# Performance work log

Hardware: AMD Instinct MI355X
Metric: run time of the kernel (lower is better)

## Reference

```python
import jax, jax.numpy as jnp
import numpy as np

L, B, S, D, H = 6, 2, 2048, 512, 8
DH = D // H
FF = 4 * D
EPS = 1e-5


def setup_inputs() -> dict:
    key = jax.random.key(0)
    ks = jax.random.split(key, 10)
    w = lambda k, shape: jax.random.normal(k, shape, jnp.float32) * 0.02
    return {
        "query": jax.random.normal(ks[0], (B, S, D), jnp.float32),
        "key": jax.random.normal(ks[1], (B, S, D), jnp.float32),
        "query_mask": jnp.ones((B, S), jnp.int32),
        "key_mask": jnp.ones((B, S), jnp.int32),
        # per-layer stacked params; conv1d(kernel=1) == linear with weight [out,in]
        "Wq": w(ks[2], (L, D, D)), "bq": jnp.zeros((L, D), jnp.float32),
        "Wk": w(ks[3], (L, D, D)), "bk": jnp.zeros((L, D), jnp.float32),
        "Wv": w(ks[4], (L, D, D)), "bv": jnp.zeros((L, D), jnp.float32),
        "Wo": w(ks[5], (L, D, D)), "bo": jnp.zeros((L, D), jnp.float32),
        "ln1_g": jnp.ones((L, D), jnp.float32), "ln1_b": jnp.zeros((L, D), jnp.float32),
        "ff_w1": w(ks[6], (L, FF, D)), "ff_b1": jnp.zeros((L, FF), jnp.float32),
        "ff_w2": w(ks[7], (L, D, FF)), "ff_b2": jnp.zeros((L, D), jnp.float32),
        "ln2_g": jnp.ones((L, D), jnp.float32), "ln2_b": jnp.zeros((L, D), jnp.float32),
    }


def _layer_norm(x, g, b):
    m = jnp.mean(x, axis=-1, keepdims=True)
    v = jnp.mean(jnp.square(x - m), axis=-1, keepdims=True)
    return (x - m) * jax.lax.rsqrt(v + EPS) * g + b


def reference(query, key, query_mask, key_mask,
              Wq, bq, Wk, bk, Wv, bv, Wo, bo,
              ln1_g, ln1_b, ff_w1, ff_b1, ff_w2, ff_b2, ln2_g, ln2_b):
    b_, s_, d_ = query.shape
    kpad = (key_mask == 0)[:, None, None, :]          # [B,1,1,K]
    qm = query_mask.astype(query.dtype)[:, :, None]    # [B,S,1]
    x = query
    for i in range(L):
        # QKV projections (conv1d kernel-size-1 == linear), split heads -> [B,H,S,DH]
        def split(t):
            return t.reshape(b_, s_, H, DH).transpose(0, 2, 1, 3)
        q = split(x @ Wq[i].T + bq[i]) * (float(DH) ** -0.5)
        k = split(key @ Wk[i].T + bk[i])
        v = split(key @ Wv[i].T + bv[i])
        attn = jnp.einsum('bhqd,bhkd->bhqk', q, k)
        attn = jnp.where(kpad, -jnp.inf, attn)
        attn = jax.nn.softmax(attn, axis=-1)
        o = jnp.einsum('bhqk,bhkd->bhqd', attn, v)
        o = o.transpose(0, 2, 1, 3).reshape(b_, s_, H * DH)
        o = (o @ Wo[i].T + bo[i]) * qm                 # output proj + query mask
        x = _layer_norm(o + x, ln1_g[i], ln1_b[i])
        h = jax.nn.leaky_relu(x @ ff_w1[i].T + ff_b1[i], 0.01)
        f = (h @ ff_w2[i].T + ff_b2[i]) * qm           # FFN mask on output
        x = _layer_norm(f + x, ln2_g[i], ln2_b[i])
    return x
```

## Files before the change

### kernel.cpp

```cpp
#include <hip/hip_runtime.h>
#include <stdint.h>

constexpr int LAYERS = 6;
constexpr int Bc = 2, Sc = 2048, Dc = 512, Hc = 8, DHc = 64, FFc = 2048;
constexpr int Mc = Bc * Sc;
constexpr int NS = 2;
constexpr int KCHUNK = Sc / NS;

typedef __attribute__((ext_vector_type(8))) __bf16 bf16x8;
typedef __attribute__((ext_vector_type(4))) __bf16 bf16x4;
typedef __attribute__((ext_vector_type(4))) float f32x4;

__device__ __forceinline__ void async_ld16(const void* g, void* lds) {
  __builtin_amdgcn_global_load_lds(
      (const __attribute__((address_space(1))) uint32_t*)g,
      (__attribute__((address_space(3))) uint32_t*)lds, 16, 0, 0);
}

__global__ __launch_bounds__(256) void cvt_all(
    const float* __restrict__ Wq, const float* __restrict__ Wo,
    const float* __restrict__ fw1, const float* __restrict__ fw2,
    const float* __restrict__ query, const float* __restrict__ key,
    __bf16* __restrict__ wq_b, __bf16* __restrict__ wo_b,
    __bf16* __restrict__ w1_b, __bf16* __restrict__ w2_b,
    __bf16* __restrict__ x_b, __bf16* __restrict__ key_b,
    float* __restrict__ x_f) {
  size_t i = ((size_t)blockIdx.x * 256 + threadIdx.x) * 4;
  constexpr size_t nW = (size_t)LAYERS * Dc * Dc;
  constexpr size_t nF = (size_t)LAYERS * FFc * Dc;
  constexpr size_t nX = (size_t)Mc * Dc;
  const float* src;
  __bf16* dst;
  float* fdst = nullptr;
  if (i < nW) { src = Wq + i; dst = wq_b + i; }
  else if (i < 2 * nW) { size_t j = i - nW; src = Wo + j; dst = wo_b + j; }
  else if (i < 2 * nW + nF) { size_t j = i - 2 * nW; src = fw1 + j; dst = w1_b + j; }
  else if (i < 2 * nW + 2 * nF) { size_t j = i - 2 * nW - nF; src = fw2 + j; dst = w2_b + j; }
  else if (i < 2 * nW + 2 * nF + nX) {
    size_t j = i - 2 * nW - 2 * nF;
    src = query + j; dst = x_b + j; fdst = x_f + j;
  } else {
    size_t j = i - 2 * nW - 2 * nF - nX;
    src = key + j; dst = key_b + j;
  }
  const float4 v = *(const float4*)src;
  bf16x4 o;
  o[0] = (__bf16)v.x; o[1] = (__bf16)v.y; o[2] = (__bf16)v.z; o[3] = (__bf16)v.w;
  *(bf16x4*)dst = o;
  if (fdst) *(float4*)fdst = v;
}

__global__ __launch_bounds__(256) void cvt_kv_kernel(const float* __restrict__ Wk,
                                                     const float* __restrict__ Wv,
                                                     __bf16* __restrict__ out) {
  size_t i = ((size_t)blockIdx.x * 256 + threadIdx.x) * 4;
  int n = (int)(i / ((size_t)Dc * Dc));
  int lyr = n >> 1, p = n & 1;
  size_t idx = i - (size_t)n * Dc * Dc;
  const float* src = (p ? Wv : Wk) + (size_t)lyr * Dc * Dc + idx;
  const float4 v = *(const float4*)src;
  bf16x4 o;
  o[0] = (__bf16)v.x; o[1] = (__bf16)v.y; o[2] = (__bf16)v.z; o[3] = (__bf16)v.w;
  *(bf16x4*)(out + i) = o;
}

__global__ __launch_bounds__(256) void kbias_kernel(const int* __restrict__ km,
                                                    float* __restrict__ kb, int n) {
  int i = blockIdx.x * 256 + threadIdx.x;
  if (i < n) kb[i] = km[i] ? 0.f : -1e30f;
}

template <int BM, int BN, int WM, int WN, int EPI>
__global__ __launch_bounds__(256) void gemm_bt(
    const __bf16* __restrict__ A, const __bf16* __restrict__ W,
    const float* __restrict__ bias, const float* __restrict__ bias2,
    float* __restrict__ outf, __bf16* __restrict__ outb,
    __bf16* __restrict__ outb2, float scale,
    int M, int N, int K, int Kstride) {
  constexpr int BK = 64;
  __shared__ __bf16 As[2][BM * BK];
  __shared__ __bf16 Bs[2][BN * BK];
  const int tid = threadIdx.x;
  const int l15 = tid & 15;
  const int lg = (tid & 63) >> 4;
  const int w = tid >> 6;
  const int wm = w >> 1, wn = w & 1;
  const int tm = blockIdx.y * BM;
  const int tn = blockIdx.x * BN;
  const int z = blockIdx.z;
  const __bf16* Ap = A + (size_t)tm * Kstride + (size_t)z * K;
  const __bf16* Wp = W + (size_t)tn * Kstride + (size_t)z * K;
  f32x4 acc[WM][WN] = {};

  auto stage = [&](int k0, int bf) {
#pragma unroll
    for (int c = 0; c < BM * 8 / 256; ++c) {
      int cc = c * 256 + tid;
      int r = cc >> 3, s = cc & 7;
      int ss = s ^ (r & 7);
      async_ld16(Ap + (size_t)r * Kstride + k0 + ss * 8, &As[bf][cc * 8]);
    }
#pragma unroll
    for (int c = 0; c < BN * 8 / 256; ++c) {
      int cc = c * 256 + tid;
      int r = cc >> 3, s = cc & 7;
      int ss = s ^ (r & 7);
      async_ld16(Wp + (size_t)r * Kstride + k0 + ss * 8, &Bs[bf][cc * 8]);
    }
  };

  const int nk = K / BK;
  stage(0, 0);
  __syncthreads();
  int buf = 0;
  for (int t = 0; t < nk; ++t) {
    if (t + 1 < nk) stage((t + 1) * BK, buf ^ 1);
    bf16x8 af[WM][2], bfr[WN][2];
#pragma unroll
    for (int i = 0; i < WM; ++i) {
      int row = wm * WM * 16 + i * 16 + l15;
#pragma unroll
      for (int kf = 0; kf < 2; ++kf)
        af[i][kf] = *(const bf16x8*)&As[buf][row * 64 + (((kf * 4 + lg) ^ (row & 7)) * 8)];
    }
#pragma unroll
    for (int j = 0; j < WN; ++j) {
      int row = wn * WN * 16 + j * 16 + l15;
#pragma unroll
      for (int kf = 0; kf < 2; ++kf)
        bfr[j][kf] = *(const bf16x8*)&Bs[buf][row * 64 + (((kf * 4 + lg) ^ (row & 7)) * 8)];
    }
#pragma unroll
    for (int kf = 0; kf < 2; ++kf)
#pragma unroll
      for (int i = 0; i < WM; ++i)
#pragma unroll
        for (int j = 0; j < WN; ++j)
          acc[i][j] = __builtin_amdgcn_mfma_f32_16x16x32_bf16(af[i][kf], bfr[j][kf], acc[i][j], 0, 0, 0);
    __syncthreads();
    buf ^= 1;
  }

  if constexpr (EPI == 6) {
    const bool isV = ((tn & 1023) >= 512);
    const int lyr = tn >> 10;
    const int b = tm >> 11;
    const int sbase = tm & (Sc - 1);
    if (isV) {
      __bf16* T = (__bf16*)&As[0][0];
#pragma unroll
      for (int i = 0; i < WM; ++i) {
#pragma unroll
        for (int j = 0; j < WN; ++j) {
          const int d = wn * WN * 16 + j * 16 + l15;
          const int dg = (tn & 511) + d;
          const float bv = bias2[lyr * 512 + dg];
          const int s0 = wm * WM * 16 + i * 16 + lg * 4;
          bf16x4 pk;
#pragma unroll
          for (int r = 0; r < 4; ++r) pk[r] = (__bf16)(acc[i][j][r] + bv);
          const int slot = (s0 >> 3) ^ (d & 7);
          *(bf16x4*)&T[d * 64 + slot * 8 + (s0 & 7)] = pk;
        }
      }
      __syncthreads();
      const int rr = tid >> 3;
      const int c8 = tid & 7;
#pragma unroll
      for (int pass = 0; pass < 4; ++pass) {
        const int d = pass * 32 + rr;
        const int slot = c8 ^ (d & 7);
        bf16x8 v8 = *(const bf16x8*)&T[d * 64 + slot * 8];
        const int dg = (tn & 511) + d;
        const int h = dg >> 6, dh = dg & 63;
        *(bf16x8*)&outb2[((((size_t)(lyr * Bc + b) * Hc + h)) * DHc + dh) * Sc +
                         sbase + c8 * 8] = v8;
      }
    } else {
#pragma unroll
      for (int i = 0; i < WM; ++i) {
#pragma unroll
        for (int j = 0; j < WN; ++j) {
          const int d = wn * WN * 16 + j * 16 + l15;
          const int dg = (tn & 511) + d;
          const float bv = bias[lyr * 512 + dg];
          const int h = dg >> 6, dh = dg & 63;
#pragma unroll
          for (int r = 0; r < 4; ++r) {
            const int s = sbase + wm * WM * 16 + i * 16 + lg * 4 + r;
            outb[((((size_t)(lyr * Bc + b) * Hc + h)) * Sc + s) * DHc + dh] =
                (__bf16)(acc[i][j][r] + bv);
          }
        }
      }
    }
    return;
  }

#pragma unroll
  for (int i = 0; i < WM; ++i) {
#pragma unroll
    for (int j = 0; j < WN; ++j) {
      const int n = tn + wn * WN * 16 + j * 16 + l15;
      float bv;
      if constexpr (EPI == 0) {
        bv = (z == 0) ? bias[n] : 0.f;
      } else {
        bv = bias[n];
      }
#pragma unroll
      for (int r = 0; r < 4; ++r) {
        const int m = tm + wm * WM * 16 + i * 16 + lg * 4 + r;
        float v = acc[i][j][r] + bv;
        if constexpr (EPI == 0) {
          outf[(size_t)z * M * N + (size_t)m * N + n] = v;
        } else if constexpr (EPI == 1) {
          int b = m >> 11, s = m & (Sc - 1);
          int h = n >> 6, dh = n & 63;
          outb[(((size_t)(b * Hc + h)) * Sc + s) * DHc + dh] = (__bf16)(v * scale);
        } else if constexpr (EPI == 4) {
          float lv = v > 0.f ? v : 0.01f * v;
          outb[(size_t)m * N + n] = (__bf16)lv;
        }
      }
    }
  }
}

__global__ __launch_bounds__(256, 5) void attn_kernel(
    const __bf16* __restrict__ q, const __bf16* __restrict__ k,
    const __bf16* __restrict__ vt, const float* __restrict__ kb,
    __bf16* __restrict__ Opart, float* __restrict__ mpart,
    float* __restrict__ lpart) {
  const int bid = blockIdx.x;
  const int o = (bid & 7) * 128 + (bid >> 3);
  const int qb = o & 31;
  const int p = o >> 5;
  const int bh = p >> 1;
  const int z = p & 1;
  const int b = bh >> 3;
  const int w = threadIdx.x >> 6;
  const int l = threadIdx.x & 63;
  const int l15 = l & 15;
  const int lg = l >> 4;
  const int tid = threadIdx.x;
  const int qbase = qb * 64 + w * 16;
  const int k0 = z * KCHUNK;

  const __bf16* qp = q + ((size_t)bh * Sc + qbase) * DHc;
  const __bf16* kp = k + (size_t)bh * Sc * DHc;
  const __bf16* vp = vt + (size_t)bh * DHc * Sc;
  const float* kbp = kb + (size_t)b * Sc;

  bf16x8 qf[2];
  qf[0] = *(const bf16x8*)(qp + l15 * DHc + lg * 8);
  qf[1] = *(const bf16x8*)(qp + l15 * DHc + 32 + lg * 8);

  bf16x8 onesf;
#pragma unroll
  for (int i = 0; i < 8; ++i) onesf[i] = (__bf16)1.0f;

  f32x4 oacc[4] = {};
  f32x4 lacc = {};
  float mr = -1e30f;

  __shared__ __bf16 Ks[2][4096];
  __shared__ __bf16 Vs[2][4096];

  auto stage = [&](int t, int bf) {
    const int kt = k0 + t * 64;
#pragma unroll
    for (int ii = 0; ii < 2; ++ii) {
      int i = ii * 256 + tid;
      int r = i >> 3;
      int bsrc = (i & 7) ^ (r & 7);
      async_ld16(kp + (size_t)(kt + r) * DHc + bsrc * 8, &Ks[bf][i * 8]);
      async_ld16(vp + (size_t)r * Sc + kt + bsrc * 8, &Vs[bf][i * 8]);
    }
  };

  stage(0, 0);
  __syncthreads();

  constexpr int NT = KCHUNK / 64;
  int buf = 0;
  for (int t = 0; t < NT; ++t) {
    const int kt = k0 + t * 64;
    if (t + 1 < NT) stage(t + 1, buf ^ 1);

    float4 mb4[4];
#pragma unroll
    for (int cb = 0; cb < 4; ++cb)
      mb4[cb] = *(const float4*)&kbp[kt + cb * 16 + lg * 4];

    f32x4 sacc[4] = {};
    __builtin_amdgcn_s_setprio(1);
#pragma unroll
    for (int kf = 0; kf < 2; ++kf) {
#pragma unroll
      for (int cb = 0; cb < 4; ++cb) {
        int row = cb * 16 + l15;
        bf16x8 kfr = *(const bf16x8*)&Ks[buf][row * 64 + (((kf * 4 + lg) ^ (row & 7)) * 8)];
        sacc[cb] = __builtin_amdgcn_mfma_f32_16x16x32_bf16(kfr, qf[kf], sacc[cb], 0, 0, 0);
      }
    }
    __builtin_amdgcn_s_setprio(0);
    sacc[0][0] += mb4[0].x; sacc[0][1] += mb4[0].y; sacc[0][2] += mb4[0].z; sacc[0][3] += mb4[0].w;
    sacc[1][0] += mb4[1].x; sacc[1][1] += mb4[1].y; sacc[1][2] += mb4[1].z; sacc[1][3] += mb4[1].w;
    sacc[2][0] += mb4[2].x; sacc[2][1] += mb4[2].y; sacc[2][2] += mb4[2].z; sacc[2][3] += mb4[2].w;
    sacc[3][0] += mb4[3].x; sacc[3][1] += mb4[3].y; sacc[3][2] += mb4[3].z; sacc[3][3] += mb4[3].w;

    float mx = sacc[0][0];
#pragma unroll
    for (int cb = 0; cb < 4; ++cb)
#pragma unroll
      for (int r = 0; r < 4; ++r) mx = fmaxf(mx, sacc[cb][r]);
    mx = fmaxf(mx, __shfl_xor(mx, 16, 64));
    mx = fmaxf(mx, __shfl_xor(mx, 32, 64));

    if (__any(mx > mr + 8.f)) {
      float mn = fmaxf(mr, mx);
      float f = __expf(mr - mn);
      mr = mn;
      float fj[4];
#pragma unroll
      for (int j = 0; j < 4; ++j) fj[j] = __shfl(f, lg * 4 + j, 64);
#pragma unroll
      for (int j = 0; j < 4; ++j) lacc[j] *= fj[j];
#pragma unroll
      for (int db = 0; db < 4; ++db)
#pragma unroll
        for (int j = 0; j < 4; ++j) oacc[db][j] *= fj[j];
    }

    unsigned pw[4][2];
#pragma unroll
    for (int cb = 0; cb < 4; ++cb) {
#pragma unroll
      for (int w2 = 0; w2 < 2; ++w2) {
        union { __bf16 h[2]; unsigned u; } cu;
        cu.h[0] = (__bf16)__expf(sacc[cb][2 * w2] - mr);
        cu.h[1] = (__bf16)__expf(sacc[cb][2 * w2 + 1] - mr);
        pw[cb][w2] = cu.u;
      }
    }

    const int srcA = ((lg & 1) * 2) * 16 + l15;
    const int srcB = srcA + 16;
    const bool hi = (lg >> 1) & 1;
#pragma unroll
    for (int kf = 0; kf < 2; ++kf) {
      unsigned t0a = __shfl((int)pw[kf * 2][0], srcA, 64);
      unsigned t0b = __shfl((int)pw[kf * 2 + 1][0], srcA, 64);
      unsigned t1a = __shfl((int)pw[kf * 2][1], srcA, 64);
      unsigned t1b = __shfl((int)pw[kf * 2 + 1][1], srcA, 64);
      unsigned t2a = __shfl((int)pw[kf * 2][0], srcB, 64);
      unsigned t2b = __shfl((int)pw[kf * 2 + 1][0], srcB, 64);
      unsigned t3a = __shfl((int)pw[kf * 2][1], srcB, 64);
      unsigned t3b = __shfl((int)pw[kf * 2 + 1][1], srcB, 64);
      union { unsigned u[4]; bf16x8 v; } pa;
      pa.u[0] = hi ? t0b : t0a;
      pa.u[1] = hi ? t1b : t1a;
      pa.u[2] = hi ? t2b : t2a;
      pa.u[3] = hi ? t3b : t3a;
      __builtin_amdgcn_s_setprio(1);
      lacc = __builtin_amdgcn_mfma_f32_16x16x32_bf16(pa.v, onesf, lacc, 0, 0, 0);
#pragma unroll
      for (int db = 0; db < 4; ++db) {
        int row = db * 16 + l15;
        bf16x8 vf = *(const bf16x8*)&Vs[buf][row * 64 + (((kf * 4 + lg) ^ (row & 7)) * 8)];
        oacc[db] = __builtin_amdgcn_mfma_f32_16x16x32_bf16(pa.v, vf, oacc[db], 0, 0, 0);
      }
      __builtin_amdgcn_s_setprio(0);
    }
    __syncthreads();
    buf ^= 1;
  }

  const size_t obase = (((size_t)(z * Bc * Hc + bh)) * Sc + qbase) * DHc;
#pragma unroll
  for (int db = 0; db < 4; ++db)
#pragma unroll
    for (int j = 0; j < 4; ++j)
      Opart[obase + (size_t)(lg * 4 + j) * DHc + db * 16 + l15] = (__bf16)oacc[db][j];
  const int row0 = (z * Bc * Hc + bh) * Sc + qbase;
  if (lg == 0) mpart[row0 + l15] = mr;
  if (l15 == 0) {
#pragma unroll
    for (int j = 0; j < 4; ++j) lpart[row0 + lg * 4 + j] = lacc[j];
  }
}

__global__ __launch_bounds__(256) void attn_combine(
    const __bf16* __restrict__ Opart, const float* __restrict__ mpart,
    const float* __restrict__ lpart, __bf16* __restrict__ out) {
  int t = blockIdx.x * 256 + threadIdx.x;
  int d = t & 63;
  int row = t >> 6;
  int bh = row >> 11, s = row & (Sc - 1);
  constexpr int RSTRIDE = Bc * Hc * Sc;
  float m0 = mpart[row], m1 = mpart[RSTRIDE + row];
  float l0 = lpart[row], l1 = lpart[RSTRIDE + row];
  float M = fmaxf(m0, m1);
  float e0 = __expf(m0 - M), e1 = __expf(m1 - M);
  float denom = e0 * l0 + e1 * l1;
  float o0 = (float)Opart[(size_t)row * DHc + d];
  float o1 = (float)Opart[((size_t)RSTRIDE + row) * DHc + d];
  float o = (e0 * o0 + e1 * o1) / denom;
  int b = bh >> 3, h = bh & 7;
  out[(((size_t)b * Sc + s)) * Dc + h * DHc + d] = (__bf16)o;
}

__global__ __launch_bounds__(256) void add_ln_kernel(
    const float* __restrict__ res, const float* __restrict__ res2,
    const int* __restrict__ rmask, const float* __restrict__ xin,
    const float* __restrict__ g, const float* __restrict__ bb,
    float* __restrict__ xo, __bf16* __restrict__ xbo) {
  const int tid = threadIdx.x;
  const int rl = tid >> 7;
  const int row = blockIdx.x * 2 + rl;
  const int ci = (tid & 127) * 4;
  const size_t base = (size_t)row * Dc + ci;
  const float4 a = *(const float4*)(res + base);
  const float4 a2 = *(const float4*)(res2 + base);
  const float4 xv = *(const float4*)(xin + base);
  const float mfac = (float)rmask[row];
  float4 v;
  v.x = (a.x + a2.x) * mfac + xv.x;
  v.y = (a.y + a2.y) * mfac + xv.y;
  v.z = (a.z + a2.z) * mfac + xv.z;
  v.w = (a.w + a2.w) * mfac + xv.w;
  float s = v.x + v.y + v.z + v.w;
#pragma unroll
  for (int d = 1; d < 64; d <<= 1) s += __shfl_xor(s, d, 64);
  __shared__ float red[4], red2[4];
  if ((tid & 63) == 0) red[tid >> 6] = s;
  __syncthreads();
  float mean = (red[rl * 2] + red[rl * 2 + 1]) * (1.0f / Dc);
  float4 dv;
  dv.x = v.x - mean; dv.y = v.y - mean; dv.z = v.z - mean; dv.w = v.w - mean;
  float qq = dv.x * dv.x + dv.y * dv.y + dv.z * dv.z + dv.w * dv.w;
#pragma unroll
  for (int d = 1; d < 64; d <<= 1) qq += __shfl_xor(qq, d, 64);
  if ((tid & 63) == 0) red2[tid >> 6] = qq;
  __syncthreads();
  float var = (red2[rl * 2] + red2[rl * 2 + 1]) * (1.0f / Dc);
  float rs = rsqrtf(var + 1e-5f);
  const float4 gv = *(const float4*)(g + ci);
  const float4 bv = *(const float4*)(bb + ci);
  float4 ov;
  ov.x = dv.x * rs * gv.x + bv.x;
  ov.y = dv.y * rs * gv.y + bv.y;
  ov.z = dv.z * rs * gv.z + bv.z;
  ov.w = dv.w * rs * gv.w + bv.w;
  *(float4*)(xo + base) = ov;
  bf16x4 ob;
  ob[0] = (__bf16)ov.x; ob[1] = (__bf16)ov.y; ob[2] = (__bf16)ov.z; ob[3] = (__bf16)ov.w;
  *(bf16x4*)(xbo + base) = ob;
}

extern "C" void kernel_launch(void* const* d_in, const int* in_sizes, int n_in,
                              void* d_out, int out_size, void* d_ws, size_t ws_size,
                              hipStream_t stream) {
  (void)in_sizes; (void)n_in; (void)out_size; (void)ws_size;
  const float* query = (const float*)d_in[0];
  const float* key   = (const float*)d_in[1];
  const int* qmask   = (const int*)d_in[2];
  const int* kmask   = (const int*)d_in[3];
  const float* Wq = (const float*)d_in[4];
  const float* bq = (const float*)d_in[5];
  const float* Wk = (const float*)d_in[6];
  const float* bk = (const float*)d_in[7];
  const float* Wv = (const float*)d_in[8];
  const float* bv = (const float*)d_in[9];
  const float* Wo = (const float*)d_in[10];
  const float* bo = (const float*)d_in[11];
  const float* ln1g = (const float*)d_in[12];
  const float* ln1b = (const float*)d_in[13];
  const float* fw1 = (const float*)d_in[14];
  const float* fb1 = (const float*)d_in[15];
  const float* fw2 = (const float*)d_in[16];
  const float* fb2 = (const float*)d_in[17];
  const float* ln2g = (const float*)d_in[18];
  const float* ln2b = (const float*)d_in[19];

  char* ws = (char*)d_ws;
  size_t off = 0;
  auto carve = [&](size_t bytes) -> void* {
    void* p = ws + off;
    off += (bytes + 255) & ~(size_t)255;
    return p;
  };
  float* x_f    = (float*)carve((size_t)Mc * Dc * 4);
  float* tmp_f  = (float*)carve((size_t)2 * Mc * Dc * 4);
  __bf16* x_b   = (__bf16*)carve((size_t)Mc * Dc * 2);
  __bf16* key_b = (__bf16*)carve((size_t)Mc * Dc * 2);
  __bf16* q_b   = (__bf16*)carve((size_t)Mc * Dc * 2);
  __bf16* at_b  = (__bf16*)carve((size_t)Mc * Dc * 2);
  __bf16* h_b   = (__bf16*)carve((size_t)Mc * FFc * 2);
  __bf16* k_all = (__bf16*)carve((size_t)LAYERS * Mc * Dc * 2);
  __bf16* vt_all= (__bf16*)carve((size_t)LAYERS * Mc * Dc * 2);
  __bf16* wq_b  = (__bf16*)carve((size_t)LAYERS * Dc * Dc * 2);
  __bf16* wkv_b = (__bf16*)carve((size_t)LAYERS * 2 * Dc * Dc * 2);
  __bf16* wo_b  = (__bf16*)carve((size_t)LAYERS * Dc * Dc * 2);
  __bf16* w1_b  = (__bf16*)carve((size_t)LAYERS * FFc * Dc * 2);
  __bf16* w2_b  = (__bf16*)carve((size_t)LAYERS * Dc * FFc * 2);
  float* ml_f   = (float*)carve((size_t)NS * Bc * Hc * Sc * 4 * 2);
  float* kb_f   = (float*)carve((size_t)Bc * Sc * 4);

  __bf16* opart_b = h_b;
  float* mpart_f = ml_f;
  float* lpart_f = ml_f + (size_t)NS * Bc * Hc * Sc;
  float* tmp2_f = tmp_f + (size_t)Mc * Dc;

  cvt_all<<<19456, 256, 0, stream>>>(Wq, Wo, fw1, fw2, query, key,
                                     wq_b, wo_b, w1_b, w2_b, x_b, key_b, x_f);
  cvt_kv_kernel<<<LAYERS * 2 * Dc * Dc / 1024, 256, 0, stream>>>(Wk, Wv, wkv_b);
  kbias_kernel<<<Bc * Sc / 256, 256, 0, stream>>>(kmask, kb_f, Bc * Sc);

  const dim3 blk(256);
  const dim3 gP64(Dc / 64, Mc / 64);
  const dim3 gOP(Dc / 64, Mc / 64, 2);
  const dim3 gFF2(Dc / 64, Mc / 64, 2);
  const dim3 gKV(LAYERS * 2 * Dc / 128, Mc / 64);
  const dim3 gFF1(FFc / 128, Mc / 64);
  const dim3 gAttn(Sc / 64 * Bc * Hc * NS);
  const dim3 gComb(Bc * Hc * Sc * DHc / 256);
  const dim3 gLN(Mc / 2);

  gemm_bt<64, 128, 2, 4, 6><<<gKV, blk, 0, stream>>>(
      key_b, wkv_b, bk, bv, nullptr, k_all, vt_all, 1.0f,
      Mc, LAYERS * 2 * Dc, Dc, Dc);

  for (int i = 0; i < LAYERS; ++i) {
    const __bf16* wq_i = wq_b + (size_t)i * Dc * Dc;
    const __bf16* wo_i = wo_b + (size_t)i * Dc * Dc;
    const __bf16* w1_i = w1_b + (size_t)i * FFc * Dc;
    const __bf16* w2_i = w2_b + (size_t)i * Dc * FFc;
    const __bf16* k_i  = k_all + (size_t)i * Mc * Dc;
    const __bf16* vt_i = vt_all + (size_t)i * Mc * Dc;

    gemm_bt<64, 64, 2, 2, 1><<<gP64, blk, 0, stream>>>(
        x_b, wq_i, bq + i * Dc, nullptr, nullptr, q_b, nullptr, 0.125f,
        Mc, Dc, Dc, Dc);
    attn_kernel<<<gAttn, blk, 0, stream>>>(q_b, k_i, vt_i, kb_f,
                                           opart_b, mpart_f, lpart_f);
    attn_combine<<<gComb, blk, 0, stream>>>(opart_b, mpart_f, lpart_f, at_b);
    gemm_bt<64, 64, 2, 2, 0><<<gOP, blk, 0, stream>>>(
        at_b, wo_i, bo + i * Dc, nullptr, tmp_f, nullptr, nullptr, 1.0f,
        Mc, Dc, Dc / 2, Dc);
    add_ln_kernel<<<gLN, blk, 0, stream>>>(tmp_f, tmp2_f, qmask, x_f,
                                           ln1g + i * Dc, ln1b + i * Dc, x_f, x_b);
    gemm_bt<64, 128, 2, 4, 4><<<gFF1, blk, 0, stream>>>(
        x_b, w1_i, fb1 + i * FFc, nullptr, nullptr, h_b, nullptr, 1.0f,
        Mc, FFc, Dc, Dc);
    gemm_bt<64, 64, 2, 2, 0><<<gFF2, blk, 0, stream>>>(
        h_b, w2_i, fb2 + i * Dc, nullptr, tmp_f, nullptr, nullptr, 1.0f,
        Mc, Dc, FFc / 2, FFc);
    add_ln_kernel<<<gLN, blk, 0, stream>>>(tmp_f, tmp2_f, qmask, x_f,
                                           ln2g + i * Dc, ln2b + i * Dc, x_f, x_b);
  }
  hipMemcpyAsync(d_out, x_f, (size_t)Mc * Dc * 4, hipMemcpyDeviceToDevice, stream);
}
```

Before: 789.2 us.

## Fuse Q projection into attention kernel and vectorize attention combine

Removes the separate Q-projection GEMM by computing each wave's 16x64 Q tile inside the attention kernel with MFMAs directly from x and the per-head Wq slice, then shuffling it into operand layout. This eliminates a kernel launch and the Q write/read round trip per layer, at the cost of recomputing Q in both key-split blocks and reading Wq/x without LDS staging. The combine kernel now processes 8 contiguous elements per thread with 16-byte loads/stores and a reciprocal instead of per-element division.

Result: slower. 916.8 us (+16.2%).

```diff
diff --git a/kernel.cpp b/kernel.cpp
--- a/kernel.cpp
+++ b/kernel.cpp
@@ -214,10 +214,6 @@
         float v = acc[i][j][r] + bv;
         if constexpr (EPI == 0) {
           outf[(size_t)z * M * N + (size_t)m * N + n] = v;
-        } else if constexpr (EPI == 1) {
-          int b = m >> 11, s = m & (Sc - 1);
-          int h = n >> 6, dh = n & 63;
-          outb[(((size_t)(b * Hc + h)) * Sc + s) * DHc + dh] = (__bf16)(v * scale);
         } else if constexpr (EPI == 4) {
           float lv = v > 0.f ? v : 0.01f * v;
           outb[(size_t)m * N + n] = (__bf16)lv;
@@ -228,7 +224,8 @@
 }
 
 __global__ __launch_bounds__(256, 5) void attn_kernel(
-    const __bf16* __restrict__ q, const __bf16* __restrict__ k,
+    const __bf16* __restrict__ xq, const __bf16* __restrict__ wq,
+    const float* __restrict__ bq, const __bf16* __restrict__ k,
     const __bf16* __restrict__ vt, const float* __restrict__ kb,
     __bf16* __restrict__ Opart, float* __restrict__ mpart,
     float* __restrict__ lpart) {
@@ -239,6 +236,7 @@
   const int bh = p >> 1;
   const int z = p & 1;
   const int b = bh >> 3;
+  const int h = bh & 7;
   const int w = threadIdx.x >> 6;
   const int l = threadIdx.x & 63;
   const int l15 = l & 15;
@@ -247,22 +245,9 @@
   const int qbase = qb * 64 + w * 16;
   const int k0 = z * KCHUNK;
 
-  const __bf16* qp = q + ((size_t)bh * Sc + qbase) * DHc;
   const __bf16* kp = k + (size_t)bh * Sc * DHc;
   const __bf16* vp = vt + (size_t)bh * DHc * Sc;
   const float* kbp = kb + (size_t)b * Sc;
-
-  bf16x8 qf[2];
-  qf[0] = *(const bf16x8*)(qp + l15 * DHc + lg * 8);
-  qf[1] = *(const bf16x8*)(qp + l15 * DHc + 32 + lg * 8);
-
-  bf16x8 onesf;
-#pragma unroll
-  for (int i = 0; i < 8; ++i) onesf[i] = (__bf16)1.0f;
-
-  f32x4 oacc[4] = {};
-  f32x4 lacc = {};
-  float mr = -1e30f;
 
   __shared__ __bf16 Ks[2][4096];
   __shared__ __bf16 Vs[2][4096];
@@ -280,6 +265,64 @@
   };
 
   stage(0, 0);
+
+  const int srcA = ((lg & 1) * 2) * 16 + l15;
+  const int srcB = srcA + 16;
+  const bool hi = (lg >> 1) & 1;
+
+  f32x4 qacc[4] = {};
+  {
+    const __bf16* xrow = xq + ((size_t)(b * Sc + qbase + l15)) * Dc;
+    const __bf16* wqh = wq + ((size_t)(h * DHc)) * Dc;
+#pragma unroll
+    for (int ks = 0; ks < 16; ++ks) {
+      bf16x8 bfrag = *(const bf16x8*)(xrow + ks * 32 + lg * 8);
+#pragma unroll
+      for (int dt = 0; dt < 4; ++dt) {
+        bf16x8 afrag = *(const bf16x8*)(wqh + (size_t)(dt * 16 + l15) * Dc + ks * 32 + lg * 8);
+        qacc[dt] = __builtin_amdgcn_mfma_f32_16x16x32_bf16(afrag, bfrag, qacc[dt], 0, 0, 0);
+      }
+    }
+  }
+  unsigned pk[4][2];
+#pragma unroll
+  for (int dt = 0; dt < 4; ++dt) {
+    const float4 bq4 = *(const float4*)&bq[h * DHc + dt * 16 + lg * 4];
+    union { __bf16 hh[2]; unsigned u; } cu;
+    cu.hh[0] = (__bf16)((qacc[dt][0] + bq4.x) * 0.125f);
+    cu.hh[1] = (__bf16)((qacc[dt][1] + bq4.y) * 0.125f);
+    pk[dt][0] = cu.u;
+    cu.hh[0] = (__bf16)((qacc[dt][2] + bq4.z) * 0.125f);
+    cu.hh[1] = (__bf16)((qacc[dt][3] + bq4.w) * 0.125f);
+    pk[dt][1] = cu.u;
+  }
+  bf16x8 qf[2];
+#pragma unroll
+  for (int kf = 0; kf < 2; ++kf) {
+    unsigned a0 = __shfl((int)pk[kf * 2][0], srcA, 64);
+    unsigned a1 = __shfl((int)pk[kf * 2][1], srcA, 64);
+    unsigned a2 = __shfl((int)pk[kf * 2][0], srcB, 64);
+    unsigned a3 = __shfl((int)pk[kf * 2][1], srcB, 64);
+    unsigned b0 = __shfl((int)pk[kf * 2 + 1][0], srcA, 64);
+    unsigned b1 = __shfl((int)pk[kf * 2 + 1][1], srcA, 64);
+    unsigned b2 = __shfl((int)pk[kf * 2 + 1][0], srcB, 64);
+    unsigned b3 = __shfl((int)pk[kf * 2 + 1][1], srcB, 64);
+    union { unsigned u[4]; bf16x8 v; } qq;
+    qq.u[0] = hi ? b0 : a0;
+    qq.u[1] = hi ? b1 : a1;
+    qq.u[2] = hi ? b2 : a2;
+    qq.u[3] = hi ? b3 : a3;
+    qf[kf] = qq.v;
+  }
+
+  bf16x8 onesf;
+#pragma unroll
+  for (int i = 0; i < 8; ++i) onesf[i] = (__bf16)1.0f;
+
+  f32x4 oacc[4] = {};
+  f32x4 lacc = {};
+  float mr = -1e30f;
+
   __syncthreads();
 
   constexpr int NT = KCHUNK / 64;
@@ -338,16 +381,13 @@
     for (int cb = 0; cb < 4; ++cb) {
 #pragma unroll
       for (int w2 = 0; w2 < 2; ++w2) {
-        union { __bf16 h[2]; unsigned u; } cu;
-        cu.h[0] = (__bf16)__expf(sacc[cb][2 * w2] - mr);
-        cu.h[1] = (__bf16)__expf(sacc[cb][2 * w2 + 1] - mr);
+        union { __bf16 hh[2]; unsigned u; } cu;
+        cu.hh[0] = (__bf16)__expf(sacc[cb][2 * w2] - mr);
+        cu.hh[1] = (__bf16)__expf(sacc[cb][2 * w2 + 1] - mr);
         pw[cb][w2] = cu.u;
       }
     }
 
-    const int srcA = ((lg & 1) * 2) * 16 + l15;
-    const int srcB = srcA + 16;
-    const bool hi = (lg >> 1) & 1;
 #pragma unroll
     for (int kf = 0; kf < 2; ++kf) {
       unsigned t0a = __shfl((int)pw[kf * 2][0], srcA, 64);
@@ -395,20 +435,23 @@
     const __bf16* __restrict__ Opart, const float* __restrict__ mpart,
     const float* __restrict__ lpart, __bf16* __restrict__ out) {
   int t = blockIdx.x * 256 + threadIdx.x;
-  int d = t & 63;
-  int row = t >> 6;
+  int g = t & 7;
+  int row = t >> 3;
   int bh = row >> 11, s = row & (Sc - 1);
   constexpr int RSTRIDE = Bc * Hc * Sc;
   float m0 = mpart[row], m1 = mpart[RSTRIDE + row];
   float l0 = lpart[row], l1 = lpart[RSTRIDE + row];
   float M = fmaxf(m0, m1);
   float e0 = __expf(m0 - M), e1 = __expf(m1 - M);
-  float denom = e0 * l0 + e1 * l1;
-  float o0 = (float)Opart[(size_t)row * DHc + d];
-  float o1 = (float)Opart[((size_t)RSTRIDE + row) * DHc + d];
-  float o = (e0 * o0 + e1 * o1) / denom;
+  float inv = 1.0f / (e0 * l0 + e1 * l1);
+  bf16x8 o0 = *(const bf16x8*)&Opart[(size_t)row * DHc + g * 8];
+  bf16x8 o1 = *(const bf16x8*)&Opart[((size_t)RSTRIDE + row) * DHc + g * 8];
+  bf16x8 r;
+#pragma unroll
+  for (int e = 0; e < 8; ++e)
+    r[e] = (__bf16)((e0 * (float)o0[e] + e1 * (float)o1[e]) * inv);
   int b = bh >> 3, h = bh & 7;
-  out[(((size_t)b * Sc + s)) * Dc + h * DHc + d] = (__bf16)o;
+  *(bf16x8*)&out[(((size_t)b * Sc + s)) * Dc + h * DHc + g * 8] = r;
 }
 
 __global__ __launch_bounds__(256) void add_ln_kernel(
@@ -495,7 +538,6 @@
   float* tmp_f  = (float*)carve((size_t)2 * Mc * Dc * 4);
   __bf16* x_b   = (__bf16*)carve((size_t)Mc * Dc * 2);
   __bf16* key_b = (__bf16*)carve((size_t)Mc * Dc * 2);
-  __bf16* q_b   = (__bf16*)carve((size_t)Mc * Dc * 2);
   __bf16* at_b  = (__bf16*)carve((size_t)Mc * Dc * 2);
   __bf16* h_b   = (__bf16*)carve((size_t)Mc * FFc * 2);
   __bf16* k_all = (__bf16*)carve((size_t)LAYERS * Mc * Dc * 2);
@@ -519,13 +561,12 @@
   kbias_kernel<<<Bc * Sc / 256, 256, 0, stream>>>(kmask, kb_f, Bc * Sc);
 
   const dim3 blk(256);
-  const dim3 gP64(Dc / 64, Mc / 64);
   const dim3 gOP(Dc / 64, Mc / 64, 2);
   const dim3 gFF2(Dc / 64, Mc / 64, 2);
   const dim3 gKV(LAYERS * 2 * Dc / 128, Mc / 64);
   const dim3 gFF1(FFc / 128, Mc / 64);
   const dim3 gAttn(Sc / 64 * Bc * Hc * NS);
-  const dim3 gComb(Bc * Hc * Sc * DHc / 256);
+  const dim3 gComb(Bc * Hc * Sc * 8 / 256);
   const dim3 gLN(Mc / 2);
 
   gemm_bt<64, 128, 2, 4, 6><<<gKV, blk, 0, stream>>>(
@@ -540,11 +581,8 @@
     const __bf16* k_i  = k_all + (size_t)i * Mc * Dc;
     const __bf16* vt_i = vt_all + (size_t)i * Mc * Dc;
 
-    gemm_bt<64, 64, 2, 2, 1><<<gP64, blk, 0, stream>>>(
-        x_b, wq_i, bq + i * Dc, nullptr, nullptr, q_b, nullptr, 0.125f,
-        Mc, Dc, Dc, Dc);
-    attn_kernel<<<gAttn, blk, 0, stream>>>(q_b, k_i, vt_i, kb_f,
-                                           opart_b, mpart_f, lpart_f);
+    attn_kernel<<<gAttn, blk, 0, stream>>>(x_b, wq_i, bq + i * Dc, k_i, vt_i,
+                                           kb_f, opart_b, mpart_f, lpart_f);
     attn_combine<<<gComb, blk, 0, stream>>>(opart_b, mpart_f, lpart_f, at_b);
     gemm_bt<64, 64, 2, 2, 0><<<gOP, blk, 0, stream>>>(
         at_b, wo_i, bo + i * Dc, nullptr, tmp_f, nullptr, nullptr, 1.0f,
```
